# Kernel optimization log

Measured on AMD Instinct MI355X. Metric: run time of the kernel, lower is better.

The kernel has to match this reference:

```python
import jax, jax.numpy as jnp
import numpy as np

B, S, D, N = 4, 2048, 1024, 256
BLK = 16                       # b = sqrt(state_dim)
DFF = int(8 / 3 * D)           # 2730, SwiGLU default
EPS = 1e-6


def setup_inputs() -> dict:
    key = jax.random.key(0)
    ks = jax.random.split(key, 12)
    rn = lambda k, shape, s=0.02: jax.random.normal(k, shape, jnp.float32) * s
    return {
        "x": jax.random.normal(ks[0], (B, S, D), jnp.float32),
        "L_skew": rn(ks[1], (BLK, BLK, BLK), 0.01),
        "R_skew": rn(ks[2], (BLK, BLK, BLK), 0.01),
        "Wg": rn(ks[3], (2 * BLK, D)), "bg": jnp.zeros((2 * BLK,), jnp.float32),
        "WB": rn(ks[4], (N, D)), "bB": jnp.zeros((N,), jnp.float32),
        "WC": rn(ks[5], (D, N)), "bC": jnp.zeros((D,), jnp.float32),
        "norm1_w": jnp.ones((D,), jnp.float32),
        "norm2_w": jnp.ones((D,), jnp.float32),
        "w1": rn(ks[6], (DFF, D)), "w2": rn(ks[7], (DFF, D)), "w3": rn(ks[8], (D, DFF)),
    }


def cayley(skew):
    # Q = (I + A)^{-1} (I - A), A skew-symmetric -> Q orthogonal
    A = skew - jnp.swapaxes(skew, -2, -1)
    I = jnp.eye(A.shape[-1], dtype=A.dtype)
    return jnp.linalg.solve(I + A, I - A)


def rmsnorm(x, w):
    rms = jnp.sqrt(jnp.mean(x * x, axis=-1, keepdims=True) + EPS)
    return w * x / rms


def reference(x, L_skew, R_skew, Wg, bg, WB, bB, WC, bC, norm1_w, norm2_w, w1, w2, w3):
    xs = rmsnorm(x, norm1_w)
    L_Q = cayley(L_skew)  # (b,b,b)
    R_Q = cayley(R_skew)

    # per-step input-dependent quantities, computed in one batched GEMM each
    gates = jax.nn.sigmoid(jnp.einsum('bsd,gd->bsg', xs, Wg) + bg)  # (B,S,2b)
    alpha, beta = gates[..., :BLK], gates[..., BLK:]
    Bx = jnp.einsum('bsd,nd->bsn', xs, WB) + bB                      # (B,S,N)

    def step(h, inp):
        a, be, bx = inp                       # (B,b),(B,b),(B,N)
        hb = h.reshape(-1, BLK, BLK)          # block view of state
        hr = jnp.einsum('cij,Bcj->Bci', R_Q, hb) * be[:, :, None]
        hp = jnp.swapaxes(hr, 1, 2)           # perm P_b (block transpose)
        hl = jnp.einsum('cij,Bcj->Bci', L_Q, hp) * a[:, :, None]
        h_new = jnp.swapaxes(hl, 1, 2).reshape(-1, N) + bx  # inv perm + B x_t
        return h_new, h_new

    h0 = jnp.zeros((x.shape[0], N), x.dtype)
    _, hs = jax.lax.scan(
        step, h0,
        (alpha.transpose(1, 0, 2), beta.transpose(1, 0, 2), Bx.transpose(1, 0, 2)))
    hs = hs.transpose(1, 0, 2)                                       # (B,S,N)
    y = jnp.einsum('bsn,dn->bsd', hs, WC) + bC

    x = x + y
    xn = rmsnorm(x, norm2_w)
    ff = jnp.einsum('bsf,df->bsd',
                    jax.nn.silu(jnp.einsum('bsd,fd->bsf', xn, w1)) *
                    jnp.einsum('bsd,fd->bsf', xn, w2), w3)
    return x + ff
```

## Files before the change

### kernel.cpp

```cpp
#include <hip/hip_runtime.h>
#include <hip/hip_bf16.h>

#define S_LEN  2048
#define BATCH  4
#define DIM    1024
#define NSTATE 256
#define DFF    2730
#define DFFP   2752
#define DFQ    2816
#define NROWS  (BATCH * S_LEN)
#define LC     32
#define WARM   48
#define NBG    384

typedef __attribute__((ext_vector_type(8))) short bf16x8;
typedef __attribute__((ext_vector_type(4))) float f32x4;

__device__ __forceinline__ float bf2f(ushort u) {
    return __uint_as_float(((unsigned int)u) << 16);
}
__device__ __forceinline__ ushort f2bf(float f) {
    unsigned int u = __float_as_uint(f);
    u += 0x7fffu + ((u >> 16) & 1u);
    return (ushort)(u >> 16);
}

__device__ __forceinline__ void gld_lds16(const ushort* g, ushort* l) {
    __builtin_amdgcn_global_load_lds(
        (const __attribute__((address_space(1))) unsigned int*)g,
        (__attribute__((address_space(3))) unsigned int*)l,
        16, 0, 0);
}


__global__ __launch_bounds__(256) void f2b_kernel(
    const float* __restrict__ src, ushort* __restrict__ dst, int n4)
{
    for (int i = blockIdx.x * 256 + threadIdx.x; i < n4; i += gridDim.x * 256) {
        float4 v = *(const float4*)(src + i * 4);
        ushort4 o;
        o.x = f2bf(v.x); o.y = f2bf(v.y); o.z = f2bf(v.z); o.w = f2bf(v.w);
        *(ushort4*)(dst + i * 4) = o;
    }
}

__global__ __launch_bounds__(256) void f2b_padrow_kernel(
    const float* __restrict__ src, ushort* __restrict__ dst, int rows_src)
{
    const int row = blockIdx.x, t = threadIdx.x;
    ushort4 o = {0, 0, 0, 0};
    if (row < rows_src) {
        float4 v = *(const float4*)(src + (size_t)row * DIM + t * 4);
        o.x = f2bf(v.x); o.y = f2bf(v.y); o.z = f2bf(v.z); o.w = f2bf(v.w);
    }
    *(ushort4*)(dst + (size_t)row * DIM + t * 4) = o;
}

__global__ __launch_bounds__(256) void pack_wbg_kernel(
    const float* __restrict__ WB, const float* __restrict__ Wg,
    ushort* __restrict__ dst)
{
    const int row = blockIdx.x, t = threadIdx.x;
    ushort4 o = {0, 0, 0, 0};
    const float* src = nullptr;
    if (row < NSTATE) src = WB + (size_t)row * DIM;
    else if (row < NSTATE + 32) src = Wg + (size_t)(row - NSTATE) * DIM;
    if (src) {
        float4 v = *(const float4*)(src + t * 4);
        o.x = f2bf(v.x); o.y = f2bf(v.y); o.z = f2bf(v.z); o.w = f2bf(v.w);
    }
    *(ushort4*)(dst + (size_t)row * DIM + t * 4) = o;
}

__global__ __launch_bounds__(256) void pad_w3_kernel(
    const float* __restrict__ w3, ushort* __restrict__ w3p)
{
    const int col = blockIdx.x * 256 + threadIdx.x;
    const int row = blockIdx.y;
    if (col >= DFFP) return;
    ushort v = 0;
    if (col < DFF) v = f2bf(w3[(size_t)row * DFF + col]);
    w3p[(size_t)row * DFFP + col] = v;
}

__global__ __launch_bounds__(256) void cayley_kernel(
    const float* __restrict__ Lsk, const float* __restrict__ Rsk,
    float* __restrict__ QL, float* __restrict__ QR)
{
    __shared__ float Ms[16][17];
    __shared__ float Rh[16][17];
    const int m = blockIdx.x;
    const float* src = (m < 16) ? (Lsk + m * 256) : (Rsk + (m - 16) * 256);
    const int t = threadIdx.x;
    const int i = t >> 4, j = t & 15;
    float a = src[i * 16 + j] - src[j * 16 + i];
    float eye = (i == j) ? 1.f : 0.f;
    Ms[i][j] = eye + a;
    Rh[i][j] = eye - a;
    __syncthreads();
    for (int k = 0; k < 16; ++k) {
        float f = Ms[i][k] / Ms[k][k];
        __syncthreads();
        if (i != k) {
            Ms[i][j] -= f * Ms[k][j];
            Rh[i][j] -= f * Rh[k][j];
        }
        __syncthreads();
    }
    float q = Rh[i][j] / Ms[i][i];
    float* dst = (m < 16) ? (QL + m * 256) : (QR + (m - 16) * 256);
    dst[i * 16 + j] = q;
}

__global__ __launch_bounds__(256) void rms_kernel(
    const float* __restrict__ xin, const float* __restrict__ nw,
    ushort* __restrict__ xo)
{
    __shared__ float part[4];
    __shared__ float invs;
    const int row = blockIdx.x, t = threadIdx.x;
    float4 xv = *(const float4*)(xin + (size_t)row * DIM + t * 4);
    float ss = xv.x * xv.x + xv.y * xv.y + xv.z * xv.z + xv.w * xv.w;
    for (int off = 32; off > 0; off >>= 1) ss += __shfl_down(ss, off, 64);
    if ((t & 63) == 0) part[t >> 6] = ss;
    __syncthreads();
    if (t == 0) {
        float tot = part[0] + part[1] + part[2] + part[3];
        invs = 1.f / sqrtf(tot / (float)DIM + 1e-6f);
    }
    __syncthreads();
    float inv = invs;
    float4 wv = *(const float4*)(nw + t * 4);
    ushort4 ov;
    ov.x = f2bf(wv.x * xv.x * inv);
    ov.y = f2bf(wv.y * xv.y * inv);
    ov.z = f2bf(wv.z * xv.z * inv);
    ov.w = f2bf(wv.w * xv.w * inv);
    *(ushort4*)(xo + (size_t)row * DIM + t * 4) = ov;
}

__global__ __launch_bounds__(256) void scan_win_kernel(
    const float* __restrict__ QL, const float* __restrict__ QR,
    const float* __restrict__ gates, const float* __restrict__ Bx,
    ushort* __restrict__ hs)
{
    __shared__ float Hs[256];
    __shared__ float Us[256];
    const int chunk = blockIdx.x, b = blockIdx.y, t = threadIdx.x;
    const int hi = t >> 4, lo = t & 15;
    float Rrow[16], Lrow[16];
    #pragma unroll
    for (int k = 0; k < 16; ++k) {
        Rrow[k] = QR[hi * 256 + lo * 16 + k];
        Lrow[k] = QL[lo * 256 + hi * 16 + k];
    }
    Hs[t] = 0.f;
    __syncthreads();
    const int wstart = chunk * LC;
    const int s0 = (wstart >= WARM) ? (wstart - WARM) : 0;
    const int send = wstart + LC;
    const float* gb = gates + (size_t)b * S_LEN * 32;
    const float* xb = Bx + (size_t)b * S_LEN * NSTATE;
    ushort* hb = hs + (size_t)b * S_LEN * NSTATE;
    float beta  = gb[s0 * 32 + 16 + hi];
    float alpha = gb[s0 * 32 + lo];
    float bx    = xb[s0 * NSTATE + t];
    for (int s = s0; s < send; ++s) {
        float betaN = 0.f, alphaN = 0.f, bxN = 0.f;
        if (s + 1 < send) {
            betaN  = gb[(s + 1) * 32 + 16 + hi];
            alphaN = gb[(s + 1) * 32 + lo];
            bxN    = xb[(s + 1) * NSTATE + t];
        }
        float acc = 0.f;
        #pragma unroll
        for (int k = 0; k < 16; ++k) acc += Rrow[k] * Hs[hi * 16 + k];
        Us[t] = beta * acc;
        __syncthreads();
        float acc2 = 0.f;
        #pragma unroll
        for (int k = 0; k < 16; ++k) acc2 += Lrow[k] * Us[k * 16 + lo];
        float h = alpha * acc2 + bx;
        Hs[t] = h;
        if (s >= wstart) hb[s * NSTATE + t] = f2bf(h);
        beta = betaN; alpha = alphaN; bx = bxN;
        __syncthreads();
    }
}

__global__ __launch_bounds__(256) void gemm_async(
    const ushort* __restrict__ A, int lda,
    const ushort* __restrict__ B, int ldb,
    int K, int ldc,
    const float* __restrict__ bias,
    const float* __restrict__ resF,
    float* __restrict__ outF)
{
    __shared__ ushort As[128 * 64];
    __shared__ ushort Bs[128 * 64];
    const int tid = threadIdx.x;
    const int m0 = blockIdx.y * 128, n0 = blockIdx.x * 128;
    const int w = tid >> 6, lane = tid & 63;
    const int wm = (w >> 1) * 64, wn = (w & 1) * 64;
    const int lr = lane & 15, quad = lane >> 4;
    const int rx = lr & 7;
    f32x4 acc[4][4];
    #pragma unroll
    for (int i = 0; i < 4; ++i)
        #pragma unroll
        for (int j = 0; j < 4; ++j) acc[i][j] = (f32x4){0.f, 0.f, 0.f, 0.f};
    const int srow = tid >> 3;
    const int scol = (((tid & 7) ^ (srow & 7)) * 8);
    const ushort* ga = A + (size_t)(m0 + srow) * lda + scol;
    const ushort* gb = B + (size_t)(n0 + srow) * ldb + scol;
    for (int kt = 0; kt < K; kt += 64) {
        #pragma unroll
        for (int p = 0; p < 4; ++p) {
            gld_lds16(ga + (size_t)(p * 32) * lda + kt, &As[p * 2048 + tid * 8]);
            gld_lds16(gb + (size_t)(p * 32) * ldb + kt, &Bs[p * 2048 + tid * 8]);
        }
        __syncthreads();
        #pragma unroll
        for (int s = 0; s < 2; ++s) {
            const int cg = ((s * 4 + quad) ^ rx) * 8;
            bf16x8 af[4], bfr[4];
            #pragma unroll
            for (int f = 0; f < 4; ++f) {
                af[f]  = *(const bf16x8*)&As[(wm + f * 16 + lr) * 64 + cg];
                bfr[f] = *(const bf16x8*)&Bs[(wn + f * 16 + lr) * 64 + cg];
            }
            #pragma unroll
            for (int i = 0; i < 4; ++i)
                #pragma unroll
                for (int j = 0; j < 4; ++j)
                    acc[i][j] = __builtin_amdgcn_mfma_f32_16x16x32_bf16(
                        af[i], bfr[j], acc[i][j], 0, 0, 0);
        }
        __syncthreads();
    }
    #pragma unroll
    for (int i = 0; i < 4; ++i) {
        int row = m0 + wm + i * 16 + quad * 4;
        #pragma unroll
        for (int j = 0; j < 4; ++j) {
            int col = n0 + wn + j * 16 + lr;
            float bv = bias ? bias[col] : 0.f;
            #pragma unroll
            for (int r = 0; r < 4; ++r) {
                size_t idx = (size_t)(row + r) * ldc + col;
                float v = acc[i][j][r] + bv;
                if (resF) v += resF[idx];
                outF[idx] = v;
            }
        }
    }
}

__global__ __launch_bounds__(256) void gemm_bxg(
    const ushort* __restrict__ A,
    const ushort* __restrict__ WBG,
    const float* __restrict__ bB, const float* __restrict__ bg,
    float* __restrict__ Bx, float* __restrict__ gates)
{
    __shared__ ushort As[128 * 64];
    __shared__ ushort Bs[128 * 64];
    const int tid = threadIdx.x;
    const int m0 = blockIdx.y * 128, n0 = blockIdx.x * 128;
    const int w = tid >> 6, lane = tid & 63;
    const int wm = (w >> 1) * 64, wn = (w & 1) * 64;
    const int lr = lane & 15, quad = lane >> 4;
    const int rx = lr & 7;
    f32x4 acc[4][4];
    #pragma unroll
    for (int i = 0; i < 4; ++i)
        #pragma unroll
        for (int j = 0; j < 4; ++j) acc[i][j] = (f32x4){0.f, 0.f, 0.f, 0.f};
    const int srow = tid >> 3;
    const int scol = (((tid & 7) ^ (srow & 7)) * 8);
    const ushort* ga = A   + (size_t)(m0 + srow) * DIM + scol;
    const ushort* gb = WBG + (size_t)(n0 + srow) * DIM + scol;
    for (int kt = 0; kt < DIM; kt += 64) {
        #pragma unroll
        for (int p = 0; p < 4; ++p) {
            gld_lds16(ga + (size_t)(p * 32) * DIM + kt, &As[p * 2048 + tid * 8]);
            gld_lds16(gb + (size_t)(p * 32) * DIM + kt, &Bs[p * 2048 + tid * 8]);
        }
        __syncthreads();
        #pragma unroll
        for (int s = 0; s < 2; ++s) {
            const int cg = ((s * 4 + quad) ^ rx) * 8;
            bf16x8 af[4], bfr[4];
            #pragma unroll
            for (int f = 0; f < 4; ++f) {
                af[f]  = *(const bf16x8*)&As[(wm + f * 16 + lr) * 64 + cg];
                bfr[f] = *(const bf16x8*)&Bs[(wn + f * 16 + lr) * 64 + cg];
            }
            #pragma unroll
            for (int i = 0; i < 4; ++i)
                #pragma unroll
                for (int j = 0; j < 4; ++j)
                    acc[i][j] = __builtin_amdgcn_mfma_f32_16x16x32_bf16(
                        af[i], bfr[j], acc[i][j], 0, 0, 0);
        }
        __syncthreads();
    }
    #pragma unroll
    for (int i = 0; i < 4; ++i) {
        int row = m0 + wm + i * 16 + quad * 4;
        #pragma unroll
        for (int j = 0; j < 4; ++j) {
            int col = n0 + wn + j * 16 + lr;
            #pragma unroll
            for (int r = 0; r < 4; ++r) {
                float v = acc[i][j][r];
                if (col < NSTATE) {
                    Bx[(size_t)(row + r) * NSTATE + col] = v + bB[col];
                } else if (col < NSTATE + 32) {
                    int g = col - NSTATE;
                    gates[(size_t)(row + r) * 32 + g] =
                        1.f / (1.f + expf(-(v + bg[g])));
                }
            }
        }
    }
}

__global__ __launch_bounds__(256, 2) void ffn_gemm(
    const ushort* __restrict__ A,
    const ushort* __restrict__ B1,
    const ushort* __restrict__ B2,
    ushort* __restrict__ pb)
{
    __shared__ ushort As [128 * 64];
    __shared__ ushort B1s[128 * 64];
    __shared__ ushort B2s[128 * 64];
    const int tid = threadIdx.x;
    const int m0 = blockIdx.y * 128, n0 = blockIdx.x * 128;
    const int w = tid >> 6, lane = tid & 63;
    const int wm = (w >> 1) * 64, wn = (w & 1) * 64;
    const int lr = lane & 15, quad = lane >> 4;
    const int rx = lr & 7;
    f32x4 acc1[4][4], acc2[4][4];
    #pragma unroll
    for (int i = 0; i < 4; ++i)
        #pragma unroll
        for (int j = 0; j < 4; ++j) {
            acc1[i][j] = (f32x4){0.f, 0.f, 0.f, 0.f};
            acc2[i][j] = (f32x4){0.f, 0.f, 0.f, 0.f};
        }
    const int srow = tid >> 3;
    const int scol = (((tid & 7) ^ (srow & 7)) * 8);
    const ushort* ga  = A  + (size_t)(m0 + srow) * DIM + scol;
    const ushort* gb1 = B1 + (size_t)(n0 + srow) * DIM + scol;
    const ushort* gb2 = B2 + (size_t)(n0 + srow) * DIM + scol;
    for (int kt = 0; kt < DIM; kt += 64) {
        #pragma unroll
        for (int p = 0; p < 4; ++p) {
            gld_lds16(ga  + (size_t)(p * 32) * DIM + kt, &As [p * 2048 + tid * 8]);
            gld_lds16(gb1 + (size_t)(p * 32) * DIM + kt, &B1s[p * 2048 + tid * 8]);
            gld_lds16(gb2 + (size_t)(p * 32) * DIM + kt, &B2s[p * 2048 + tid * 8]);
        }
        __syncthreads();
        #pragma unroll
        for (int s = 0; s < 2; ++s) {
            const int cg = ((s * 4 + quad) ^ rx) * 8;
            bf16x8 af[4], b1f[4], b2f[4];
            #pragma unroll
            for (int f = 0; f < 4; ++f) {
                af[f]  = *(const bf16x8*)&As [(wm + f * 16 + lr) * 64 + cg];
                b1f[f] = *(const bf16x8*)&B1s[(wn + f * 16 + lr) * 64 + cg];
                b2f[f] = *(const bf16x8*)&B2s[(wn + f * 16 + lr) * 64 + cg];
            }
            #pragma unroll
            for (int i = 0; i < 4; ++i)
                #pragma unroll
                for (int j = 0; j < 4; ++j) {
                    acc1[i][j] = __builtin_amdgcn_mfma_f32_16x16x32_bf16(
                        af[i], b1f[j], acc1[i][j], 0, 0, 0);
                    acc2[i][j] = __builtin_amdgcn_mfma_f32_16x16x32_bf16(
                        af[i], b2f[j], acc2[i][j], 0, 0, 0);
                }
        }
        __syncthreads();
    }
    #pragma unroll
    for (int i = 0; i < 4; ++i) {
        int row = m0 + wm + i * 16 + quad * 4;
        #pragma unroll
        for (int j = 0; j < 4; ++j) {
            int col = n0 + wn + j * 16 + lr;
            if (col < DFFP) {
                #pragma unroll
                for (int r = 0; r < 4; ++r) {
                    float v1 = acc1[i][j][r];
                    float v2 = acc2[i][j][r];
                    float p = v1 / (1.f + expf(-v1)) * v2;
                    pb[(size_t)(row + r) * DFFP + col] = f2bf(p);
                }
            }
        }
    }
}

extern "C" void kernel_launch(void* const* d_in, const int* in_sizes, int n_in,
                              void* d_out, int out_size, void* d_ws, size_t ws_size,
                              hipStream_t stream) {
    const float* x   = (const float*)d_in[0];
    const float* Lsk = (const float*)d_in[1];
    const float* Rsk = (const float*)d_in[2];
    const float* Wg  = (const float*)d_in[3];
    const float* bg  = (const float*)d_in[4];
    const float* WB  = (const float*)d_in[5];
    const float* bB  = (const float*)d_in[6];
    const float* WC  = (const float*)d_in[7];
    const float* bC  = (const float*)d_in[8];
    const float* n1w = (const float*)d_in[9];
    const float* n2w = (const float*)d_in[10];
    const float* w1  = (const float*)d_in[11];
    const float* w2  = (const float*)d_in[12];
    const float* w3  = (const float*)d_in[13];
    float* out = (float*)d_out;

    char* wp = (char*)d_ws;
    auto carve = [&](size_t bytes) -> char* {
        char* p = wp;
        wp += (bytes + 255) & ~(size_t)255;
        return p;
    };
    float*  QL    = (float*)carve(16 * 256 * 4);
    float*  QR    = (float*)carve(16 * 256 * 4);
    ushort* WBGb  = (ushort*)carve((size_t)NBG * DIM * 2);
    ushort* WCb   = (ushort*)carve((size_t)DIM * NSTATE * 2);
    ushort* w1p   = (ushort*)carve((size_t)DFQ * DIM * 2);
    ushort* w2p   = (ushort*)carve((size_t)DFQ * DIM * 2);
    ushort* w3p   = (ushort*)carve((size_t)DIM * DFFP * 2);
    ushort* xs    = (ushort*)carve((size_t)NROWS * DIM * 2);
    float*  x2    = (float*)carve((size_t)NROWS * DIM * 4);
    ushort* pb    = (ushort*)carve((size_t)NROWS * DFFP * 2);
    char*   scr   = carve((size_t)16 << 20);
    float*  gates = (float*)scr;
    float*  Bx    = (float*)(scr + (1 << 21));
    ushort* hs    = (ushort*)(scr + (11u << 20));
    ushort* xn    = xs;

    cayley_kernel<<<32, 256, 0, stream>>>(Lsk, Rsk, QL, QR);
    pack_wbg_kernel<<<NBG, 256, 0, stream>>>(WB, Wg, WBGb);
    f2b_kernel<<<256, 256, 0, stream>>>(WC, WCb, DIM * NSTATE / 4);
    f2b_padrow_kernel<<<DFQ, 256, 0, stream>>>(w1, w1p, DFF);
    f2b_padrow_kernel<<<DFQ, 256, 0, stream>>>(w2, w2p, DFF);
    pad_w3_kernel<<<dim3(11, DIM), 256, 0, stream>>>(w3, w3p);
    rms_kernel<<<NROWS, 256, 0, stream>>>(x, n1w, xs);
    gemm_bxg<<<dim3(3, 64), 256, 0, stream>>>(xs, WBGb, bB, bg, Bx, gates);
    scan_win_kernel<<<dim3(S_LEN / LC, BATCH), 256, 0, stream>>>(QL, QR, gates, Bx, hs);
    gemm_async<<<dim3(8, 64), 256, 0, stream>>>(hs, NSTATE, WCb, NSTATE, NSTATE, DIM,
                                                bC, x, x2);
    rms_kernel<<<NROWS, 256, 0, stream>>>(x2, n2w, xn);
    ffn_gemm<<<dim3(DFQ / 128, 64), 256, 0, stream>>>(xn, w1p, w2p, pb);
    gemm_async<<<dim3(8, 64), 256, 0, stream>>>(pb, DFFP, w3p, DFFP, DFFP, DIM,
                                                nullptr, x2, out);
}
```

Before: 451.2 us.

## Interleave w1/w2 rows and rewrite FFN up-GEMM as pipelined 256x256 8-wave kernel

Packs w1 and w2 into one row-interleaved bf16 matrix so the gate and up projections run as a single GEMM, with SiLU*mul applied in the epilogue by pairing adjacent columns through a lane shuffle. The FFN up-projection kernel becomes a 512-thread, 256x256-tile kernel with double-buffered LDS (128KB), staged async global-to-LDS loads interleaved with MFMA phases, explicit waitcnt/barriers and setprio. The aim is more reuse per tile and overlap of memory traffic with matrix math, at the cost of high register and LDS pressure (likely one block per CU) and intricate sync correctness.

```diff
diff --git a/kernel.cpp b/kernel.cpp
--- a/kernel.cpp
+++ b/kernel.cpp
@@ -12,6 +12,7 @@
 #define LC     32
 #define WARM   48
 #define NBG    384
+#define FFN_NT (DIM / 64)
 
 typedef __attribute__((ext_vector_type(8))) short bf16x8;
 typedef __attribute__((ext_vector_type(4))) float f32x4;
@@ -32,7 +33,6 @@
         16, 0, 0);
 }
 
-
 __global__ __launch_bounds__(256) void f2b_kernel(
     const float* __restrict__ src, ushort* __restrict__ dst, int n4)
 {
@@ -44,13 +44,16 @@
     }
 }
 
-__global__ __launch_bounds__(256) void f2b_padrow_kernel(
-    const float* __restrict__ src, ushort* __restrict__ dst, int rows_src)
+__global__ __launch_bounds__(256) void pack_w12_kernel(
+    const float* __restrict__ w1, const float* __restrict__ w2,
+    ushort* __restrict__ dst)
 {
     const int row = blockIdx.x, t = threadIdx.x;
+    const int srow = row >> 1;
+    const float* src = (row & 1) ? w2 : w1;
     ushort4 o = {0, 0, 0, 0};
-    if (row < rows_src) {
-        float4 v = *(const float4*)(src + (size_t)row * DIM + t * 4);
+    if (srow < DFF) {
+        float4 v = *(const float4*)(src + (size_t)srow * DIM + t * 4);
         o.x = f2bf(v.x); o.y = f2bf(v.y); o.z = f2bf(v.z); o.w = f2bf(v.w);
     }
     *(ushort4*)(dst + (size_t)row * DIM + t * 4) = o;
@@ -325,77 +328,153 @@
     }
 }
 
-__global__ __launch_bounds__(256, 2) void ffn_gemm(
+__global__ __launch_bounds__(512, 2) void ffn_gemm8(
     const ushort* __restrict__ A,
-    const ushort* __restrict__ B1,
-    const ushort* __restrict__ B2,
+    const ushort* __restrict__ W12,
     ushort* __restrict__ pb)
 {
-    __shared__ ushort As [128 * 64];
-    __shared__ ushort B1s[128 * 64];
-    __shared__ ushort B2s[128 * 64];
+    __shared__ ushort sm[65536];
     const int tid = threadIdx.x;
-    const int m0 = blockIdx.y * 128, n0 = blockIdx.x * 128;
-    const int w = tid >> 6, lane = tid & 63;
-    const int wm = (w >> 1) * 64, wn = (w & 1) * 64;
+    const int m0 = blockIdx.y * 256, n0 = blockIdx.x * 256;
+    const int wid = tid >> 6, lane = tid & 63;
+    const int wr = wid >> 2, wc = wid & 3;
     const int lr = lane & 15, quad = lane >> 4;
     const int rx = lr & 7;
-    f32x4 acc1[4][4], acc2[4][4];
-    #pragma unroll
-    for (int i = 0; i < 4; ++i)
+    const int srow = tid >> 3;
+    const int scol = ((tid & 7) ^ (srow & 7)) * 8;
+
+    f32x4 acc[8][4];
+    #pragma unroll
+    for (int i = 0; i < 8; ++i)
+        #pragma unroll
+        for (int j = 0; j < 4; ++j) acc[i][j] = (f32x4){0.f, 0.f, 0.f, 0.f};
+
+    const ushort* gA = A   + (size_t)(m0 + srow) * DIM + scol;
+    const ushort* gB = W12 + (size_t)(n0 + srow) * DIM + scol;
+
+    auto STAGE = [&](int pi, int which, int t) {
+        const ushort* src = (which < 2 ? gA : gB)
+                            + (size_t)((which & 1) * 128) * DIM + t * 64;
+        ushort* dst = &sm[pi * 32768 + which * 8192 + tid * 8];
+        gld_lds16(src, dst);
+        gld_lds16(src + (size_t)64 * DIM, dst + 4096);
+    };
+    const int aBase = wr * 8192;
+    const int bBase = 16384 + (wc >> 1) * 8192 + ((wc & 1) * 64) * 64;
+    auto LDA4 = [&](bf16x8 (*d)[2], int half, int pi) {
+        #pragma unroll
+        for (int f = 0; f < 4; ++f) {
+            const int ro = pi * 32768 + aBase + (half * 64 + f * 16 + lr) * 64;
+            d[f][0] = *(const bf16x8*)&sm[ro + ((quad ^ rx) * 8)];
+            d[f][1] = *(const bf16x8*)&sm[ro + (((4 + quad) ^ rx) * 8)];
+        }
+    };
+    auto LDB2 = [&](bf16x8 (*d)[2], int half, int pi) {
+        #pragma unroll
+        for (int g = 0; g < 2; ++g) {
+            const int ro = pi * 32768 + bBase + ((half * 2 + g) * 16 + lr) * 64;
+            d[g][0] = *(const bf16x8*)&sm[ro + ((quad ^ rx) * 8)];
+            d[g][1] = *(const bf16x8*)&sm[ro + (((4 + quad) ^ rx) * 8)];
+        }
+    };
+
+    STAGE(0, 0, 0); STAGE(0, 1, 0); STAGE(0, 2, 0); STAGE(0, 3, 0);
+    STAGE(1, 0, 1); STAGE(1, 1, 1);
+    asm volatile("s_waitcnt vmcnt(4)");
+    __builtin_amdgcn_s_barrier();
+
+    bf16x8 a0[4][2], a1[4][2], b0[2][2], b1[2][2];
+
+    #pragma unroll 2
+    for (int t = 0; t < FFN_NT; ++t) {
+        const int pi = t & 1;
+        LDA4(a0, 0, pi);
+        LDB2(b0, 0, pi);
+        if (t + 1 < FFN_NT) STAGE(pi ^ 1, 2, t + 1);
+        asm volatile("s_waitcnt lgkmcnt(8)");
+        __builtin_amdgcn_s_barrier();
+        asm volatile("s_waitcnt lgkmcnt(0)");
+        __builtin_amdgcn_sched_barrier(0);
+        __builtin_amdgcn_s_setprio(1);
+        #pragma unroll
+        for (int f = 0; f < 4; ++f)
+            #pragma unroll
+            for (int g = 0; g < 2; ++g) {
+                acc[f][g] = __builtin_amdgcn_mfma_f32_16x16x32_bf16(
+                    a0[f][0], b0[g][0], acc[f][g], 0, 0, 0);
+                acc[f][g] = __builtin_amdgcn_mfma_f32_16x16x32_bf16(
+                    a0[f][1], b0[g][1], acc[f][g], 0, 0, 0);
+            }
+        __builtin_amdgcn_s_setprio(0);
+        __builtin_amdgcn_s_barrier();
+        LDA4(a1, 1, pi);
+        if (t + 1 < FFN_NT) STAGE(pi ^ 1, 3, t + 1);
+        __builtin_amdgcn_s_barrier();
+        asm volatile("s_waitcnt lgkmcnt(0)");
+        __builtin_amdgcn_sched_barrier(0);
+        __builtin_amdgcn_s_setprio(1);
+        #pragma unroll
+        for (int f = 0; f < 4; ++f)
+            #pragma unroll
+            for (int g = 0; g < 2; ++g) {
+                acc[4 + f][g] = __builtin_amdgcn_mfma_f32_16x16x32_bf16(
+                    a1[f][0], b0[g][0], acc[4 + f][g], 0, 0, 0);
+                acc[4 + f][g] = __builtin_amdgcn_mfma_f32_16x16x32_bf16(
+                    a1[f][1], b0[g][1], acc[4 + f][g], 0, 0, 0);
+            }
+        __builtin_amdgcn_s_setprio(0);
+        __builtin_amdgcn_s_barrier();
+        LDB2(b1, 1, pi);
+        if (t + 2 < FFN_NT) STAGE(pi, 0, t + 2);
+        __builtin_amdgcn_s_barrier();
+        asm volatile("s_waitcnt lgkmcnt(0)");
+        __builtin_amdgcn_sched_barrier(0);
+        __builtin_amdgcn_s_setprio(1);
+        #pragma unroll
+        for (int f = 0; f < 4; ++f)
+            #pragma unroll
+            for (int g = 0; g < 2; ++g) {
+                acc[4 + f][2 + g] = __builtin_amdgcn_mfma_f32_16x16x32_bf16(
+                    a1[f][0], b1[g][0], acc[4 + f][2 + g], 0, 0, 0);
+                acc[4 + f][2 + g] = __builtin_amdgcn_mfma_f32_16x16x32_bf16(
+                    a1[f][1], b1[g][1], acc[4 + f][2 + g], 0, 0, 0);
+            }
+        __builtin_amdgcn_s_setprio(0);
+        __builtin_amdgcn_s_barrier();
+        if (t + 2 < FFN_NT) STAGE(pi, 1, t + 2);
+        __builtin_amdgcn_s_barrier();
+        __builtin_amdgcn_s_setprio(1);
+        #pragma unroll
+        for (int f = 0; f < 4; ++f)
+            #pragma unroll
+            for (int g = 0; g < 2; ++g) {
+                acc[f][2 + g] = __builtin_amdgcn_mfma_f32_16x16x32_bf16(
+                    a0[f][0], b1[g][0], acc[f][2 + g], 0, 0, 0);
+                acc[f][2 + g] = __builtin_amdgcn_mfma_f32_16x16x32_bf16(
+                    a0[f][1], b1[g][1], acc[f][2 + g], 0, 0, 0);
+            }
+        __builtin_amdgcn_s_setprio(0);
+        if (t == FFN_NT - 2) asm volatile("s_waitcnt vmcnt(0)");
+        else                 asm volatile("s_waitcnt vmcnt(4)");
+        __builtin_amdgcn_s_barrier();
+    }
+
+    #pragma unroll
+    for (int i = 0; i < 8; ++i) {
+        const int row = m0 + wr * 128 + i * 16 + quad * 4;
         #pragma unroll
         for (int j = 0; j < 4; ++j) {
-            acc1[i][j] = (f32x4){0.f, 0.f, 0.f, 0.f};
-            acc2[i][j] = (f32x4){0.f, 0.f, 0.f, 0.f};
-        }
-    const int srow = tid >> 3;
-    const int scol = (((tid & 7) ^ (srow & 7)) * 8);
-    const ushort* ga  = A  + (size_t)(m0 + srow) * DIM + scol;
-    const ushort* gb1 = B1 + (size_t)(n0 + srow) * DIM + scol;
-    const ushort* gb2 = B2 + (size_t)(n0 + srow) * DIM + scol;
-    for (int kt = 0; kt < DIM; kt += 64) {
-        #pragma unroll
-        for (int p = 0; p < 4; ++p) {
-            gld_lds16(ga  + (size_t)(p * 32) * DIM + kt, &As [p * 2048 + tid * 8]);
-            gld_lds16(gb1 + (size_t)(p * 32) * DIM + kt, &B1s[p * 2048 + tid * 8]);
-            gld_lds16(gb2 + (size_t)(p * 32) * DIM + kt, &B2s[p * 2048 + tid * 8]);
-        }
-        __syncthreads();
-        #pragma unroll
-        for (int s = 0; s < 2; ++s) {
-            const int cg = ((s * 4 + quad) ^ rx) * 8;
-            bf16x8 af[4], b1f[4], b2f[4];
-            #pragma unroll
-            for (int f = 0; f < 4; ++f) {
-                af[f]  = *(const bf16x8*)&As [(wm + f * 16 + lr) * 64 + cg];
-                b1f[f] = *(const bf16x8*)&B1s[(wn + f * 16 + lr) * 64 + cg];
-                b2f[f] = *(const bf16x8*)&B2s[(wn + f * 16 + lr) * 64 + cg];
-            }
-            #pragma unroll
-            for (int i = 0; i < 4; ++i)
-                #pragma unroll
-                for (int j = 0; j < 4; ++j) {
-                    acc1[i][j] = __builtin_amdgcn_mfma_f32_16x16x32_bf16(
-                        af[i], b1f[j], acc1[i][j], 0, 0, 0);
-                    acc2[i][j] = __builtin_amdgcn_mfma_f32_16x16x32_bf16(
-                        af[i], b2f[j], acc2[i][j], 0, 0, 0);
-                }
-        }
-        __syncthreads();
-    }
-    #pragma unroll
-    for (int i = 0; i < 4; ++i) {
-        int row = m0 + wm + i * 16 + quad * 4;
-        #pragma unroll
-        for (int j = 0; j < 4; ++j) {
-            int col = n0 + wn + j * 16 + lr;
-            if (col < DFFP) {
-                #pragma unroll
-                for (int r = 0; r < 4; ++r) {
-                    float v1 = acc1[i][j][r];
-                    float v2 = acc2[i][j][r];
-                    float p = v1 / (1.f + expf(-v1)) * v2;
-                    pb[(size_t)(row + r) * DFFP + col] = f2bf(p);
+            const int col = n0 + wc * 64 + j * 16 + lr;
+            #pragma unroll
+            for (int r = 0; r < 4; ++r) {
+                float v  = acc[i][j][r];
+                float vp = __shfl_xor(v, 1, 64);
+                if (!(lr & 1)) {
+                    const int oc = col >> 1;
+                    if (oc < DFFP) {
+                        float p = v / (1.f + expf(-v)) * vp;
+                        pb[(size_t)(row + r) * DFFP + oc] = f2bf(p);
+                    }
                 }
             }
         }
@@ -431,8 +510,7 @@
     float*  QR    = (float*)carve(16 * 256 * 4);
     ushort* WBGb  = (ushort*)carve((size_t)NBG * DIM * 2);
     ushort* WCb   = (ushort*)carve((size_t)DIM * NSTATE * 2);
-    ushort* w1p   = (ushort*)carve((size_t)DFQ * DIM * 2);
-    ushort* w2p   = (ushort*)carve((size_t)DFQ * DIM * 2);
+    ushort* w12   = (ushort*)carve((size_t)2 * DFQ * DIM * 2);
     ushort* w3p   = (ushort*)carve((size_t)DIM * DFFP * 2);
     ushort* xs    = (ushort*)carve((size_t)NROWS * DIM * 2);
     float*  x2    = (float*)carve((size_t)NROWS * DIM * 4);
@@ -446,8 +524,7 @@
     cayley_kernel<<<32, 256, 0, stream>>>(Lsk, Rsk, QL, QR);
     pack_wbg_kernel<<<NBG, 256, 0, stream>>>(WB, Wg, WBGb);
     f2b_kernel<<<256, 256, 0, stream>>>(WC, WCb, DIM * NSTATE / 4);
-    f2b_padrow_kernel<<<DFQ, 256, 0, stream>>>(w1, w1p, DFF);
-    f2b_padrow_kernel<<<DFQ, 256, 0, stream>>>(w2, w2p, DFF);
+    pack_w12_kernel<<<2 * DFQ, 256, 0, stream>>>(w1, w2, w12);
     pad_w3_kernel<<<dim3(11, DIM), 256, 0, stream>>>(w3, w3p);
     rms_kernel<<<NROWS, 256, 0, stream>>>(x, n1w, xs);
     gemm_bxg<<<dim3(3, 64), 256, 0, stream>>>(xs, WBGb, bB, bg, Bx, gates);
@@ -455,7 +532,7 @@
     gemm_async<<<dim3(8, 64), 256, 0, stream>>>(hs, NSTATE, WCb, NSTATE, NSTATE, DIM,
                                                 bC, x, x2);
     rms_kernel<<<NROWS, 256, 0, stream>>>(x2, n2w, xn);
-    ffn_gemm<<<dim3(DFQ / 128, 64), 256, 0, stream>>>(xn, w1p, w2p, pb);
+    ffn_gemm8<<<dim3(2 * DFQ / 256, NROWS / 256), 512, 0, stream>>>(xn, w12, pb);
     gemm_async<<<dim3(8, 64), 256, 0, stream>>>(pb, DFFP, w3p, DFFP, DFFP, DIM,
                                                 nullptr, x2, out);
 }
```

Result: slower. 498.7 us (+10.5%).
